# Kernel optimization log

Hardware: AMD Instinct MI355X
Metric: run time of the kernel (lower is better)

The kernel has to match this reference:

```python
import jax, jax.numpy as jnp
import numpy as np

IMG = 800.0
OUT_H = OUT_W = 7
SR = 2  # sampling_ratio
SCALES = (0.25, 0.125, 0.0625, 0.03125)
CANON_SCALE = 224.0
CANON_LVL = 4.0
K_MIN, K_MAX = 2, 5


def _make_boxes(key, n):
    k1, k2, k3 = jax.random.split(key, 3)
    c = jax.random.uniform(k1, (n, 2), minval=0.0, maxval=IMG)          # centers (cx, cy)
    logs = jax.random.uniform(k2, (n, 2), minval=np.log(32.0), maxval=np.log(512.0))
    wh = jnp.exp(logs)                                                   # sizes 32..512 px
    x1y1 = jnp.clip(c - wh / 2, 0.0, IMG - 2.0)
    x2y2 = jnp.clip(c + wh / 2, x1y1 + 1.0, IMG)
    return jnp.concatenate([x1y1, x2y2], axis=1)  # [n,4] xyxy


def setup_inputs() -> dict:
    key = jax.random.key(0)
    ks = jax.random.split(key, 6)
    return {
        "feat0": jax.random.normal(ks[0], (2, 256, 200, 200), jnp.float32),
        "feat1": jax.random.normal(ks[1], (2, 256, 100, 100), jnp.float32),
        "feat2": jax.random.normal(ks[2], (2, 256, 50, 50), jnp.float32),
        "feat3": jax.random.normal(ks[3], (2, 256, 25, 25), jnp.float32),
        "boxes0": _make_boxes(ks[4], 256),
        "boxes1": _make_boxes(ks[5], 256),
    }


def _roi_align(feat_bhwc, rois, scale):
    """torchvision roi_align (aligned=False). feat_bhwc: [B,H,W,C], rois: [R,5] (b,x1,y1,x2,y2)."""
    B, H, W, C = feat_bhwc.shape
    R = rois.shape[0]
    bidx = rois[:, 0].astype(jnp.int32)
    x1, y1, x2, y2 = (rois[:, i] * scale for i in (1, 2, 3, 4))
    roi_w = jnp.maximum(x2 - x1, 1.0)
    roi_h = jnp.maximum(y2 - y1, 1.0)
    bin_w = roi_w / OUT_W
    bin_h = roi_h / OUT_H
    # sample grid: (g + 0.5)/SR bins == bin_index + (sub + 0.5)/SR
    gy = (jnp.arange(OUT_H * SR, dtype=feat_bhwc.dtype) + 0.5) / SR
    gx = (jnp.arange(OUT_W * SR, dtype=feat_bhwc.dtype) + 0.5) / SR
    y = y1[:, None] + gy[None, :] * bin_h[:, None]  # [R, GY]
    x = x1[:, None] + gx[None, :] * bin_w[:, None]  # [R, GX]

    def prep(c, size):
        valid = ((c > -1.0) & (c < size)).astype(feat_bhwc.dtype)
        c = jnp.clip(c, 0.0)
        lo = jnp.minimum(jnp.floor(c).astype(jnp.int32), size - 1)
        hi = jnp.minimum(lo + 1, size - 1)
        frac = jnp.where(lo >= size - 1, 0.0, c - lo.astype(feat_bhwc.dtype))
        return lo, hi, frac, valid

    yl, yh, fy, vy = prep(y, H)
    xl, xh, fx, vx = prep(x, W)
    b = bidx[:, None, None]

    def g(yi, xi):  # gather -> [R, GY, GX, C]
        return feat_bhwc[b, yi[:, :, None], xi[:, None, :]]

    wy = fy[:, :, None, None]
    wx = fx[:, None, :, None]
    val = (g(yl, xl) * (1 - wy) * (1 - wx) + g(yl, xh) * (1 - wy) * wx
           + g(yh, xl) * wy * (1 - wx) + g(yh, xh) * wy * wx)
    val = val * (vy[:, :, None, None] * vx[:, None, :, None])
    val = val.reshape(R, OUT_H, SR, OUT_W, SR, C).mean(axis=(2, 4))  # avg over SRxSR samples
    return jnp.transpose(val, (0, 3, 1, 2))  # [R, C, OUT_H, OUT_W]


def _forward(feat0, feat1, feat2, feat3, boxes0, boxes1):
    feats = [feat0, feat1, feat2, feat3]
    boxes = [boxes0, boxes1]
    # convert_to_roi_format
    ids = jnp.concatenate([jnp.full((b.shape[0], 1), i, dtype=b.dtype) for i, b in enumerate(boxes)], 0)
    cat = jnp.concatenate(boxes, 0)  # [R,4]
    rois = jnp.concatenate([ids, cat], 1)  # [R,5]
    # LevelMapper (FPN eq. 1)
    area = (cat[:, 2] - cat[:, 0]) * (cat[:, 3] - cat[:, 1])
    s = jnp.sqrt(area)
    tgt = jnp.floor(CANON_LVL + jnp.log2(s / CANON_SCALE) + 1e-6)
    levels = (jnp.clip(tgt, K_MIN, K_MAX) - K_MIN).astype(jnp.int32)  # [R] in 0..3
    per = [_roi_align(jnp.transpose(f, (0, 2, 3, 1)), rois, sc) for f, sc in zip(feats, SCALES)]
    stacked = jnp.stack(per)  # [L, R, C, 7, 7]
    R = rois.shape[0]
    return stacked[levels, jnp.arange(R)]  # route each roi to its level


def reference(feat0, feat1, feat2, feat3, boxes0, boxes1):
    return _forward(feat0, feat1, feat2, feat3, boxes0, boxes1)
```

## Files before the change

### kernel.cpp

```cpp
#include <hip/hip_runtime.h>


#define NBINS 49
#define NCH 256
#define RPB 256
#define CPW 16

__global__ __launch_bounds__(256) void msroi_kernel(
    const float* __restrict__ f0, const float* __restrict__ f1,
    const float* __restrict__ f2, const float* __restrict__ f3,
    const float* __restrict__ boxes0, const float* __restrict__ boxes1,
    float* __restrict__ out)
{
    const int r    = blockIdx.x;
    const int q    = blockIdx.y;
    const int tid  = threadIdx.x;
    const int lane = tid & 63;
    const int wid  = tid >> 6;
    const int c0   = q * 64 + wid * CPW;

    const int b = (r < RPB) ? 0 : 1;
    const float* bx = (b == 0) ? (boxes0 + (size_t)r * 4)
                               : (boxes1 + (size_t)(r - RPB) * 4);
    const float x1b = bx[0], y1b = bx[1], x2b = bx[2], y2b = bx[3];

    const float area = (x2b - x1b) * (y2b - y1b);
    const float s    = sqrtf(area);
    const float tgt  = floorf(4.0f + log2f(s / 224.0f) + 1e-6f);
    const float lvlf = fminf(fmaxf(tgt, 2.0f), 5.0f);
    const int   lvl  = (int)lvlf - 2;

    int H, W;
    const float* feat;
    float scale;
    switch (lvl) {
      case 0:  feat = f0; H = 200; W = 200; scale = 0.25f;    break;
      case 1:  feat = f1; H = 100; W = 100; scale = 0.125f;   break;
      case 2:  feat = f2; H = 50;  W = 50;  scale = 0.0625f;  break;
      default: feat = f3; H = 25;  W = 25;  scale = 0.03125f; break;
    }
    const int HW = H * W;

    const float x1 = x1b * scale, y1 = y1b * scale;
    const float x2 = x2b * scale, y2 = y2b * scale;
    const float roi_w = fmaxf(x2 - x1, 1.0f);
    const float roi_h = fmaxf(y2 - y1, 1.0f);
    const float bin_w = roi_w / 7.0f;
    const float bin_h = roi_h / 7.0f;

    const bool active = (lane < NBINS);
    const int  binid  = active ? lane : 0;
    const int  oh = binid / 7, ow = binid % 7;

    int   offs[16];
    float wts[16];
    {
      int t = 0;
      #pragma unroll
      for (int sy = 0; sy < 2; ++sy) {
        const float iy = (float)(oh * 2 + sy);
        const float yy = y1 + ((iy + 0.5f) * 0.5f) * bin_h;
        const float vy = (yy > -1.0f && yy < (float)H) ? 1.0f : 0.0f;
        const float yc = fmaxf(yy, 0.0f);
        const int   yl = min((int)yc, H - 1);
        const int   yh = min(yl + 1, H - 1);
        const float fy = (yl >= H - 1) ? 0.0f : (yc - (float)yl);
        const float ay0 = vy * (1.0f - fy), ay1 = vy * fy;
        #pragma unroll
        for (int sx = 0; sx < 2; ++sx) {
          const float ix = (float)(ow * 2 + sx);
          const float xx = x1 + ((ix + 0.5f) * 0.5f) * bin_w;
          const float vx = (xx > -1.0f && xx < (float)W) ? 1.0f : 0.0f;
          const float xc = fmaxf(xx, 0.0f);
          const int   xl = min((int)xc, W - 1);
          const int   xh = min(xl + 1, W - 1);
          const float fx = (xl >= W - 1) ? 0.0f : (xc - (float)xl);
          const float ax0 = vx * (1.0f - fx), ax1 = vx * fx;
          offs[t] = yl * W + xl;  wts[t] = ay0 * ax0;  ++t;
          offs[t] = yl * W + xh;  wts[t] = ay0 * ax1;  ++t;
          offs[t] = yh * W + xl;  wts[t] = ay1 * ax0;  ++t;
          offs[t] = yh * W + xh;  wts[t] = ay1 * ax1;  ++t;
        }
      }
      if (!active) {
        #pragma unroll
        for (int k = 0; k < 16; ++k) { offs[k] = 0; wts[k] = 0.0f; }
      }
    }

    const float* fb = feat + (size_t)b * NCH * HW + (size_t)c0 * HW;
    float* ob = out + (size_t)r * (NCH * NBINS) + (size_t)c0 * NBINS;

    #pragma unroll 2
    for (int ci = 0; ci < CPW; ++ci) {
      const float* fc = fb + (size_t)ci * HW;
      float acc = 0.0f;
      #pragma unroll
      for (int k = 0; k < 16; ++k)
        acc += wts[k] * fc[offs[k]];
      if (active)
        ob[(size_t)ci * NBINS + binid] = acc * 0.25f;
    }
}

extern "C" void kernel_launch(void* const* d_in, const int* in_sizes, int n_in,
                              void* d_out, int out_size, void* d_ws, size_t ws_size,
                              hipStream_t stream) {
    const float* f0 = (const float*)d_in[0];
    const float* f1 = (const float*)d_in[1];
    const float* f2 = (const float*)d_in[2];
    const float* f3 = (const float*)d_in[3];
    const float* b0 = (const float*)d_in[4];
    const float* b1 = (const float*)d_in[5];
    float* out = (float*)d_out;

    msroi_kernel<<<dim3(512, 4), dim3(256), 0, stream>>>(f0, f1, f2, f3, b0, b1, out);
}
```

Baseline: 267.8 us.

## Stage ROI feature patch into per-wave LDS before bilinear sampling

Each wave now loads the ROI's bounding patch of each channel from global memory into a private shared-memory buffer with coalesced row-chunk loads, then computes the 16 bilinear taps from LDS. This replaces scattered global gathers with dense loads and reuses overlapping taps. It adds a serialized per-channel load-then-compute loop with no double buffering and no unroll, and a fixed 1600-float capacity per wave that large level-0 ROIs (up to about 130x130) can exceed, risking out-of-bounds shared writes.

```diff
diff --git a/kernel.cpp b/kernel.cpp
--- a/kernel.cpp
+++ b/kernel.cpp
@@ -5,6 +5,7 @@
 #define NCH 256
 #define RPB 256
 #define CPW 16
+#define CAPF 1600
 
 __global__ __launch_bounds__(256) void msroi_kernel(
     const float* __restrict__ f0, const float* __restrict__ f1,
@@ -12,6 +13,8 @@
     const float* __restrict__ boxes0, const float* __restrict__ boxes1,
     float* __restrict__ out)
 {
+    __shared__ float regbuf[4 * CAPF + 64];
+
     const int r    = blockIdx.x;
     const int q    = blockIdx.y;
     const int tid  = threadIdx.x;
@@ -48,58 +51,95 @@
     const float bin_w = roi_w / 7.0f;
     const float bin_h = roi_h / 7.0f;
 
+    auto ycoord = [&](int i) { return y1 + (((float)i + 0.5f) * 0.5f) * bin_h; };
+    auto xcoord = [&](int i) { return x1 + (((float)i + 0.5f) * 0.5f) * bin_w; };
+
+    const int yl_min = min((int)fmaxf(ycoord(0),  0.0f), H - 1);
+    const int yl_max = min((int)fmaxf(ycoord(13), 0.0f), H - 1);
+    const int xl_min = min((int)fmaxf(xcoord(0),  0.0f), W - 1);
+    const int xl_max = min((int)fmaxf(xcoord(13), 0.0f), W - 1);
+    const int y0 = yl_min;
+    const int x0 = xl_min;
+    const int ph = min(yl_max + 1, H - 1) - y0 + 1;
+    const int pw = xl_max - x0 + 2;
+    const int pwp = pw | 1;
+
+    int lsh;
+    if      (pw <= 8)  lsh = 3;
+    else if (pw <= 16) lsh = 4;
+    else if (pw <= 32) lsh = 5;
+    else               lsh = 6;
+    const int chunk  = 1 << lsh;
+    const int rpi    = 64 >> lsh;
+    const int srow   = lane >> lsh;
+    const int scol   = lane & (chunk - 1);
+    const int nstage = (ph + rpi - 1) >> (6 - lsh);
+
     const bool active = (lane < NBINS);
     const int  binid  = active ? lane : 0;
     const int  oh = binid / 7, ow = binid % 7;
 
-    int   offs[16];
-    float wts[16];
-    {
-      int t = 0;
+    int   iA[4], iB[4];
+    float w00[4], w01[4], w10[4], w11[4];
+    #pragma unroll
+    for (int sy = 0; sy < 2; ++sy) {
+      const float yy = ycoord(oh * 2 + sy);
+      const float vy = (yy > -1.0f && yy < (float)H) ? 1.0f : 0.0f;
+      const float yc = fmaxf(yy, 0.0f);
+      const int   yl = min((int)yc, H - 1);
+      const int   yh = min(yl + 1, H - 1);
+      const float fy = (yl >= H - 1) ? 0.0f : (yc - (float)yl);
       #pragma unroll
-      for (int sy = 0; sy < 2; ++sy) {
-        const float iy = (float)(oh * 2 + sy);
-        const float yy = y1 + ((iy + 0.5f) * 0.5f) * bin_h;
-        const float vy = (yy > -1.0f && yy < (float)H) ? 1.0f : 0.0f;
-        const float yc = fmaxf(yy, 0.0f);
-        const int   yl = min((int)yc, H - 1);
-        const int   yh = min(yl + 1, H - 1);
-        const float fy = (yl >= H - 1) ? 0.0f : (yc - (float)yl);
-        const float ay0 = vy * (1.0f - fy), ay1 = vy * fy;
-        #pragma unroll
-        for (int sx = 0; sx < 2; ++sx) {
-          const float ix = (float)(ow * 2 + sx);
-          const float xx = x1 + ((ix + 0.5f) * 0.5f) * bin_w;
-          const float vx = (xx > -1.0f && xx < (float)W) ? 1.0f : 0.0f;
-          const float xc = fmaxf(xx, 0.0f);
-          const int   xl = min((int)xc, W - 1);
-          const int   xh = min(xl + 1, W - 1);
-          const float fx = (xl >= W - 1) ? 0.0f : (xc - (float)xl);
-          const float ax0 = vx * (1.0f - fx), ax1 = vx * fx;
-          offs[t] = yl * W + xl;  wts[t] = ay0 * ax0;  ++t;
-          offs[t] = yl * W + xh;  wts[t] = ay0 * ax1;  ++t;
-          offs[t] = yh * W + xl;  wts[t] = ay1 * ax0;  ++t;
-          offs[t] = yh * W + xh;  wts[t] = ay1 * ax1;  ++t;
+      for (int sx = 0; sx < 2; ++sx) {
+        const float xx = xcoord(ow * 2 + sx);
+        const float vx = (xx > -1.0f && xx < (float)W) ? 1.0f : 0.0f;
+        const float xc = fmaxf(xx, 0.0f);
+        const int   xl = min((int)xc, W - 1);
+        const float fx = (xl >= W - 1) ? 0.0f : (xc - (float)xl);
+        const int   sI = sy * 2 + sx;
+        const float vv = vy * vx * 0.25f;
+        iA[sI] = (yl - y0) * pwp + (xl - x0);
+        iB[sI] = (yh - y0) * pwp + (xl - x0);
+        w00[sI] = vv * (1.0f - fy) * (1.0f - fx);
+        w01[sI] = vv * (1.0f - fy) * fx;
+        w10[sI] = vv * fy * (1.0f - fx);
+        w11[sI] = vv * fy * fx;
+        if (!active) {
+          iA[sI] = 0; iB[sI] = 0;
+          w00[sI] = w01[sI] = w10[sI] = w11[sI] = 0.0f;
         }
-      }
-      if (!active) {
-        #pragma unroll
-        for (int k = 0; k < 16; ++k) { offs[k] = 0; wts[k] = 0.0f; }
       }
     }
 
     const float* fb = feat + (size_t)b * NCH * HW + (size_t)c0 * HW;
     float* ob = out + (size_t)r * (NCH * NBINS) + (size_t)c0 * NBINS;
+    float* wbuf = regbuf + wid * CAPF;
 
-    #pragma unroll 2
     for (int ci = 0; ci < CPW; ++ci) {
       const float* fc = fb + (size_t)ci * HW;
+
+      for (int cc = 0; cc < pw; cc += chunk) {
+        const int col = cc + scol;
+        const bool cw = (col < pw);
+        const int sxc = min(x0 + min(col, pw - 1), W - 1);
+        for (int i = 0; i < nstage; ++i) {
+          const int rr = min(i * rpi + srow, ph - 1);
+          const float v = fc[(y0 + rr) * W + sxc];
+          if (cw) wbuf[rr * pwp + col] = v;
+        }
+      }
+      asm volatile("s_waitcnt lgkmcnt(0)" ::: "memory");
+
       float acc = 0.0f;
       #pragma unroll
-      for (int k = 0; k < 16; ++k)
-        acc += wts[k] * fc[offs[k]];
-      if (active)
-        ob[(size_t)ci * NBINS + binid] = acc * 0.25f;
+      for (int sI = 0; sI < 4; ++sI) {
+        const float a0 = wbuf[iA[sI]];
+        const float a1 = wbuf[iA[sI] + 1];
+        const float b0 = wbuf[iB[sI]];
+        const float b1 = wbuf[iB[sI] + 1];
+        acc += w00[sI] * a0 + w01[sI] * a1 + w10[sI] * b0 + w11[sI] * b1;
+      }
+      if (active) ob[(size_t)ci * NBINS + binid] = acc;
     }
 }
 
```

Measured after the change: 320.7 us. +19.8%, slower.
